# Optimization experiments

Hardware: AMD Instinct MI355X
Metric: run time of the kernel (lower is better)

The kernel has to match this reference:

```python
import jax, jax.numpy as jnp
import numpy as np

V = 1024          # vocab_size
N = 500_000       # num automaton states
A = 16            # arcs per non-start state (start state has V dense arcs)
MAX_ORDER = 4     # max n-gram order -> max backoff chain length
START = 0         # start (unigram) state
B = 8192          # batch of hypotheses


def _build_automaton(seed=0):
    rng = np.random.default_rng(seed)
    num_arcs = V + (N - 1) * A
    arcs_weights = -(rng.random(num_arcs).astype(np.float32) * 8.0 + 0.05)
    to_states = rng.integers(0, N, num_arcs).astype(np.int32)
    ilabels = np.empty(num_arcs, np.int32)
    ilabels[:V] = np.arange(V, dtype=np.int32)  # start state: arc index == ilabel
    # unique sorted ilabels per non-start state
    base = rng.integers(0, V, N - 1).astype(np.int32)
    offs = np.arange(A, dtype=np.int32) * (V // A)
    ilabels[V:] = np.sort((base[:, None] + offs[None, :]) % V, axis=1).reshape(-1)
    state_start = np.empty(N, np.int32)
    state_end = np.empty(N, np.int32)
    state_start[0] = 0
    state_end[0] = V
    state_start[1:] = V + np.arange(N - 1, dtype=np.int32) * A
    state_end[1:] = state_start[1:] + A
    # state orders: start=1, rest in 2..MAX_ORDER; backoff goes to an order-(k-1) state
    order = np.empty(N, np.int64)
    order[0] = 1
    order[1:] = rng.integers(2, MAX_ORDER + 1, N - 1)
    order[1:MAX_ORDER] = np.arange(2, MAX_ORDER + 1)  # guarantee each order nonempty
    backoff_to = np.zeros(N, np.int32)               # order-2 states back off to START
    for k in range(3, MAX_ORDER + 1):
        mask = order == k
        prev = np.flatnonzero(order == k - 1)
        backoff_to[mask] = rng.choice(prev, mask.sum()).astype(np.int32)
    backoff_weights = -(rng.random(N).astype(np.float32) * 3.0)
    backoff_weights[0] = 0.0
    return dict(
        arcs_weights=jnp.asarray(arcs_weights),
        backoff_weights=jnp.asarray(backoff_weights),
        ilabels=jnp.asarray(ilabels),
        to_states=jnp.asarray(to_states),
        backoff_to_states=jnp.asarray(backoff_to),
        state_start_arcs=jnp.asarray(state_start),
        state_end_arcs=jnp.asarray(state_end),
    )


def setup_inputs() -> dict:
    key = jax.random.key(0)
    inp = _build_automaton(0)
    inp["states"] = jax.random.randint(key, (B,), 0, N, dtype=jnp.int32)
    return inp


def _advance(states, arcs_weights, backoff_weights, ilabels, to_states,
             backoff_to_states, state_start_arcs, state_end_arcs):
    b = states.shape[0]
    rows = jnp.arange(b)[:, None]
    # column V is a dump slot for masked-out scatters
    scores_e = jnp.zeros((b, V + 1), arcs_weights.dtype)
    next_e = jnp.zeros((b, V + 1), jnp.int32)
    found_e = jnp.zeros((b, V + 1), bool)
    cur = states.astype(jnp.int32)
    acc = jnp.zeros((b,), arcs_weights.dtype)  # accumulated backoff weight
    offs = jnp.arange(A, dtype=jnp.int32)
    for _ in range(MAX_ORDER - 1):  # chase backoffs down to the start state
        at_start = cur == START
        idx = state_start_arcs[cur][:, None] + offs                    # [b, A]
        valid = (idx < state_end_arcs[cur][:, None]) & (~at_start)[:, None]
        idx = jnp.where(valid, idx, 0)
        lab = ilabels[idx]                                             # [b, A]
        can = valid & ~jnp.take_along_axis(found_e, lab, axis=1)
        slot = jnp.where(can, lab, V)
        scores_e = scores_e.at[rows, slot].set(acc[:, None] + arcs_weights[idx])
        next_e = next_e.at[rows, slot].set(to_states[idx])
        found_e = found_e.at[rows, slot].set(True)
        acc = jnp.where(at_start, acc, acc + backoff_weights[cur])
        cur = jnp.where(at_start, cur, backoff_to_states[cur])
    # start state has a dense arc table: arc index == ilabel for 0..V-1
    nf = ~found_e[:, :V]
    scores = jnp.where(nf, acc[:, None] + arcs_weights[None, :V], scores_e[:, :V])
    next_states = jnp.where(nf, to_states[None, :V], next_e[:, :V])
    return scores, next_states


def reference(states, arcs_weights, backoff_weights, ilabels, to_states,
              backoff_to_states, state_start_arcs, state_end_arcs):
    return _advance(states, arcs_weights, backoff_weights, ilabels, to_states,
                    backoff_to_states, state_start_arcs, state_end_arcs)
```

## Files before the change

### kernel.cpp

```cpp
#include <hip/hip_runtime.h>

#define VOCAB 1024
#define ARCS  16
#define MAX_ORDER 4
#define CHAIN (MAX_ORDER - 1)
#define START_STATE 0
#define WAVE 64

__global__ __launch_bounds__(WAVE) void ngram_advance_kernel(
    const float* __restrict__ arcs_weights,
    const float* __restrict__ backoff_weights,
    const int*   __restrict__ ilabels,
    const int*   __restrict__ to_states,
    const int*   __restrict__ backoff_to,
    const int*   __restrict__ state_start,
    const int*   __restrict__ state_end,
    const int*   __restrict__ states,
    float*       __restrict__ out_scores,
    float*       __restrict__ out_next)
{
    __shared__ int   s_next_ov[VOCAB];
    __shared__ float s_score_ov[VOCAB];

    const int tid = threadIdx.x;
    const int b   = blockIdx.x;

    #pragma unroll
    for (int i = 0; i < VOCAB / (WAVE * 4); ++i) {
        const int v = (tid + i * WAVE) * 4;
        *(int4*)&s_next_ov[v] = make_int4(-1, -1, -1, -1);
    }

    int   cs[CHAIN];
    float ca[CHAIN];
    int   cur = states[b];
    float acc = 0.0f;
    #pragma unroll
    for (int t = 0; t < CHAIN; ++t) {
        cs[t] = cur;
        ca[t] = acc;
        if (cur != START_STATE) {
            acc += backoff_weights[cur];
            cur  = backoff_to[cur];
        }
    }
    const float accf = acc;

    const int level = tid >> 4;
    const int arc   = tid & (ARCS - 1);
    bool  ok  = false;
    int   lab = 0, ns = 0;
    float sc  = 0.0f;
    if (tid < CHAIN * ARCS) {
        const int s = (level == 0) ? cs[0] : ((level == 1) ? cs[1] : cs[2]);
        if (s != START_STATE) {
            const int st  = state_start[s];
            const int en  = state_end[s];
            const int idx = st + arc;
            if (idx < en) {
                ok  = true;
                lab = ilabels[idx];
                sc  = ((level == 0) ? ca[0] : ((level == 1) ? ca[1] : ca[2]))
                      + arcs_weights[idx];
                ns  = to_states[idx];
            }
        }
    }
    __syncthreads();

    if (ok && level == 2) { s_score_ov[lab] = sc; s_next_ov[lab] = ns; }
    __syncthreads();
    if (ok && level == 1) { s_score_ov[lab] = sc; s_next_ov[lab] = ns; }
    __syncthreads();
    if (ok && level == 0) { s_score_ov[lab] = sc; s_next_ov[lab] = ns; }
    __syncthreads();

    float* __restrict__ so = out_scores + (size_t)b * VOCAB;
    float* __restrict__ no = out_next   + (size_t)b * VOCAB;
    #pragma unroll
    for (int i = 0; i < VOCAB / (WAVE * 4); ++i) {
        const int v = (tid + i * WAVE) * 4;
        const int4   ons = *(const int4*)  &s_next_ov[v];
        const float4 osc = *(const float4*)&s_score_ov[v];
        const float4 dw  = *(const float4*)&arcs_weights[v];
        const int4   dn  = *(const int4*)  &to_states[v];
        float4 rs, rn;
        rs.x = (ons.x >= 0) ? osc.x : accf + dw.x;
        rs.y = (ons.y >= 0) ? osc.y : accf + dw.y;
        rs.z = (ons.z >= 0) ? osc.z : accf + dw.z;
        rs.w = (ons.w >= 0) ? osc.w : accf + dw.w;
        rn.x = (float)((ons.x >= 0) ? ons.x : dn.x);
        rn.y = (float)((ons.y >= 0) ? ons.y : dn.y);
        rn.z = (float)((ons.z >= 0) ? ons.z : dn.z);
        rn.w = (float)((ons.w >= 0) ? ons.w : dn.w);
        *(float4*)&so[v] = rs;
        *(float4*)&no[v] = rn;
    }
}

extern "C" void kernel_launch(void* const* d_in, const int* in_sizes, int n_in,
                              void* d_out, int out_size, void* d_ws, size_t ws_size,
                              hipStream_t stream) {
    const float* arcs_weights    = (const float*)d_in[0];
    const float* backoff_weights = (const float*)d_in[1];
    const int*   ilabels         = (const int*)d_in[2];
    const int*   to_states       = (const int*)d_in[3];
    const int*   backoff_to      = (const int*)d_in[4];
    const int*   state_start     = (const int*)d_in[5];
    const int*   state_end       = (const int*)d_in[6];
    const int*   states          = (const int*)d_in[7];

    const int B = in_sizes[7];
    float* out_scores = (float*)d_out;
    float* out_next   = out_scores + (size_t)B * VOCAB;

    ngram_advance_kernel<<<B, WAVE, 0, stream>>>(
        arcs_weights, backoff_weights, ilabels, to_states, backoff_to,
        state_start, state_end, states, out_scores, out_next);
}
```

Baseline: 19.36 us.

## Replace LDS overlay and barriers with wave-level dedup and global scatter

```diff
diff --git a/kernel.cpp b/kernel.cpp
--- a/kernel.cpp
+++ b/kernel.cpp
@@ -7,7 +7,7 @@
 #define START_STATE 0
 #define WAVE 64
 
-__global__ __launch_bounds__(WAVE) void ngram_advance_kernel(
+__global__ __launch_bounds__(WAVE, 8) void ngram_advance_kernel(
     const float* __restrict__ arcs_weights,
     const float* __restrict__ backoff_weights,
     const int*   __restrict__ ilabels,
@@ -19,82 +19,68 @@
     float*       __restrict__ out_scores,
     float*       __restrict__ out_next)
 {
-    __shared__ int   s_next_ov[VOCAB];
-    __shared__ float s_score_ov[VOCAB];
-
     const int tid = threadIdx.x;
     const int b   = blockIdx.x;
 
-    #pragma unroll
-    for (int i = 0; i < VOCAB / (WAVE * 4); ++i) {
-        const int v = (tid + i * WAVE) * 4;
-        *(int4*)&s_next_ov[v] = make_int4(-1, -1, -1, -1);
-    }
-
-    int   cs[CHAIN];
-    float ca[CHAIN];
     int   cur = states[b];
     float acc = 0.0f;
-    #pragma unroll
-    for (int t = 0; t < CHAIN; ++t) {
-        cs[t] = cur;
-        ca[t] = acc;
-        if (cur != START_STATE) {
-            acc += backoff_weights[cur];
-            cur  = backoff_to[cur];
-        }
-    }
+    const int   cs0 = cur;  const float ca0 = acc;
+    if (cur != START_STATE) { acc += backoff_weights[cur]; cur = backoff_to[cur]; }
+    const int   cs1 = cur;  const float ca1 = acc;
+    if (cur != START_STATE) { acc += backoff_weights[cur]; cur = backoff_to[cur]; }
+    const int   cs2 = cur;  const float ca2 = acc;
+    if (cur != START_STATE) { acc += backoff_weights[cur]; }
     const float accf = acc;
 
     const int level = tid >> 4;
     const int arc   = tid & (ARCS - 1);
+    int   lab = -1, ns = 0;
+    float sc  = 0.0f;
     bool  ok  = false;
-    int   lab = 0, ns = 0;
-    float sc  = 0.0f;
     if (tid < CHAIN * ARCS) {
-        const int s = (level == 0) ? cs[0] : ((level == 1) ? cs[1] : cs[2]);
+        const int   s    = (level == 0) ? cs0 : ((level == 1) ? cs1 : cs2);
+        const float cacc = (level == 0) ? ca0 : ((level == 1) ? ca1 : ca2);
         if (s != START_STATE) {
-            const int st  = state_start[s];
-            const int en  = state_end[s];
-            const int idx = st + arc;
-            if (idx < en) {
+            const int idx = state_start[s] + arc;
+            if (idx < state_end[s]) {
+                lab = ilabels[idx];
+                sc  = cacc + arcs_weights[idx];
+                ns  = to_states[idx];
                 ok  = true;
-                lab = ilabels[idx];
-                sc  = ((level == 0) ? ca[0] : ((level == 1) ? ca[1] : ca[2]))
-                      + arcs_weights[idx];
-                ns  = to_states[idx];
             }
         }
     }
-    __syncthreads();
 
-    if (ok && level == 2) { s_score_ov[lab] = sc; s_next_ov[lab] = ns; }
-    __syncthreads();
-    if (ok && level == 1) { s_score_ov[lab] = sc; s_next_ov[lab] = ns; }
-    __syncthreads();
-    if (ok && level == 0) { s_score_ov[lab] = sc; s_next_ov[lab] = ns; }
-    __syncthreads();
+    int kill = 0;
+    #pragma unroll
+    for (int k = 0; k < 2 * ARCS; ++k) {
+        const int lk = __builtin_amdgcn_readlane(lab, k);
+        if (k < ARCS) kill |= (int)(level >= 1) & (int)(lab == lk);
+        else          kill |= (int)(level == 2) & (int)(lab == lk);
+    }
+    const bool do_scatter = ok && !kill;
 
     float* __restrict__ so = out_scores + (size_t)b * VOCAB;
     float* __restrict__ no = out_next   + (size_t)b * VOCAB;
     #pragma unroll
     for (int i = 0; i < VOCAB / (WAVE * 4); ++i) {
         const int v = (tid + i * WAVE) * 4;
-        const int4   ons = *(const int4*)  &s_next_ov[v];
-        const float4 osc = *(const float4*)&s_score_ov[v];
-        const float4 dw  = *(const float4*)&arcs_weights[v];
-        const int4   dn  = *(const int4*)  &to_states[v];
+        const float4 dw = *(const float4*)&arcs_weights[v];
+        const int4   dn = *(const int4*)&to_states[v];
         float4 rs, rn;
-        rs.x = (ons.x >= 0) ? osc.x : accf + dw.x;
-        rs.y = (ons.y >= 0) ? osc.y : accf + dw.y;
-        rs.z = (ons.z >= 0) ? osc.z : accf + dw.z;
-        rs.w = (ons.w >= 0) ? osc.w : accf + dw.w;
-        rn.x = (float)((ons.x >= 0) ? ons.x : dn.x);
-        rn.y = (float)((ons.y >= 0) ? ons.y : dn.y);
-        rn.z = (float)((ons.z >= 0) ? ons.z : dn.z);
-        rn.w = (float)((ons.w >= 0) ? ons.w : dn.w);
+        rs.x = accf + dw.x;  rs.y = accf + dw.y;
+        rs.z = accf + dw.z;  rs.w = accf + dw.w;
+        rn.x = (float)dn.x;  rn.y = (float)dn.y;
+        rn.z = (float)dn.z;  rn.w = (float)dn.w;
         *(float4*)&so[v] = rs;
         *(float4*)&no[v] = rn;
+    }
+
+    asm volatile("s_waitcnt vmcnt(0)" ::: "memory");
+
+    if (do_scatter) {
+        so[lab] = sc;
+        no[lab] = (float)ns;
     }
 }
 
```

Result: slower. 20.11 us (+3.9%).
